# Performance work log

Measured on AMD Instinct MI355X. Metric: run time of the kernel, lower is better.

## Reference

```python
import jax, jax.numpy as jnp
import numpy as np

K = 10
SLOPE = 0.2
FEATS = [3, 64, 128, 256, 512, 1024]
MLP = [1024, 128, 64, 1]
B, N = 8, 2048


def setup_inputs() -> dict:
    key = jax.random.key(0)
    keys = jax.random.split(key, 32)
    inp = {"x": jax.random.normal(keys[0], (B, N, 3), dtype=jnp.float32)}
    ki = 1
    for i in range(5):
        fin, fout = 2 * FEATS[i], FEATS[i + 1]
        s = 1.0 / np.sqrt(fin)
        inp[f"w{i}"] = jax.random.uniform(keys[ki], (fin, fout), jnp.float32, -s, s); ki += 1
        inp[f"b{i}"] = jax.random.uniform(keys[ki], (fout,), jnp.float32, -s, s); ki += 1
    for i in range(3):
        fin, fout = MLP[i], MLP[i + 1]
        s = 1.0 / np.sqrt(fin)
        inp[f"m{i}w"] = jax.random.uniform(keys[ki], (fin, fout), jnp.float32, -s, s); ki += 1
        inp[f"m{i}b"] = jax.random.uniform(keys[ki], (fout,), jnp.float32, -s, s); ki += 1
    return inp


def _knn_idx(xb):
    # xb: [N, F]; squared euclidean distances, self included (dist 0)
    sq = jnp.sum(xb * xb, axis=-1)
    d2 = sq[:, None] + sq[None, :] - 2.0 * (xb @ xb.T)
    _, idx = jax.lax.top_k(-d2, K)  # [N, K] nearest (incl. self)
    return idx


def _edge_conv(x, W, b):
    # x: [B, N, F] -> [B, N, Fout]
    fin = x.shape[-1]
    W1, W2 = W[:fin], W[fin:]  # split concat([x_i, x_j - x_i]) @ W
    idx = jax.vmap(_knn_idx)(x)  # [B, N, K]
    x_j = jax.vmap(lambda xb, ib: xb[ib])(x, idx)  # [B, N, K, F]
    h_center = x @ W1 + b  # [B, N, Fout]
    diff = x_j - x[:, :, None, :]
    h = h_center[:, :, None, :] + jnp.einsum('bnkf,fo->bnko', diff, W2)
    h = jnp.where(h > 0, h, SLOPE * h)  # LeakyReLU(0.2)
    return jnp.max(h, axis=2)  # max aggregation over neighbors


def reference(x, w0, b0, w1, b1, w2, b2, w3, b3, w4, b4,
              m0w, m0b, m1w, m1b, m2w, m2b):
    ws = [(w0, b0), (w1, b1), (w2, b2), (w3, b3), (w4, b4)]
    h = x
    for W, b in ws:
        h = _edge_conv(h, W, b)
    g = jnp.max(h, axis=1)  # MaxPool1d(kernel=2048) -> global max over points: [B, 1024]
    g = g @ m0w + m0b
    g = g @ m1w + m1b
    g = g @ m2w + m2b
    return g  # [B, 1]
```

## Files before the change

### kernel.cpp

```cpp
#include <hip/hip_runtime.h>
#include <hip/hip_bf16.h>
#include <math.h>

#define BB 8
#define NN 2048
#define KK 10
#define BN (BB * NN)
#define HC 1024

typedef __attribute__((ext_vector_type(8))) short bf16x8;
typedef __attribute__((ext_vector_type(4))) float f32x4;

__device__ inline unsigned short f2bf(float f) {
    unsigned int u = __float_as_uint(f);
    unsigned int r = u + 0x7fffu + ((u >> 16) & 1u);
    return (unsigned short)(r >> 16);
}
__device__ inline float bf2f(unsigned short h) {
    return __uint_as_float((unsigned int)h << 16);
}

__device__ __forceinline__ void async16(const void* g, void* l) {
    __builtin_amdgcn_global_load_lds(
        (const __attribute__((address_space(1))) void*)g,
        (__attribute__((address_space(3))) void*)l, 16, 0, 0);
}

__global__ void xsplit3_kernel(const float* __restrict__ x,
                               unsigned short* __restrict__ hi,
                               unsigned short* __restrict__ lo,
                               float* __restrict__ sq) {
    int row = blockIdx.x * blockDim.x + threadIdx.x;
    if (row >= BN) return;
    unsigned short hbuf[32], lbuf[32];
#pragma unroll
    for (int f = 0; f < 32; ++f) { hbuf[f] = 0; lbuf[f] = 0; }
    float s = 0.f;
#pragma unroll
    for (int f = 0; f < 3; ++f) {
        float v = x[(size_t)row * 3 + f];
        s += v * v;
        unsigned short h = f2bf(v);
        hbuf[f] = h;
        lbuf[f] = f2bf(v - bf2f(h));
    }
    sq[row] = s;
#pragma unroll
    for (int f = 0; f < 32; f += 8) {
        *(uint4*)&hi[(size_t)row * 32 + f] = *(uint4*)&hbuf[f];
        *(uint4*)&lo[(size_t)row * 32 + f] = *(uint4*)&lbuf[f];
    }
}

__global__ __launch_bounds__(256) void xsplit_sq_kernel(
        const float* __restrict__ x, unsigned short* __restrict__ hi,
        unsigned short* __restrict__ lo, float* __restrict__ sq, int F) {
    int row = blockIdx.x * 4 + (threadIdx.x >> 6);
    int lane = threadIdx.x & 63;
    const float* xp = x + (size_t)row * F;
    float s = 0.f;
    for (int f = lane; f < F; f += 64) {
        float v = xp[f];
        unsigned short h = f2bf(v);
        hi[(size_t)row * F + f] = h;
        lo[(size_t)row * F + f] = f2bf(v - bf2f(h));
        s += v * v;
    }
#pragma unroll
    for (int off = 32; off > 0; off >>= 1) s += __shfl_down(s, off);
    if (lane == 0) sq[row] = s;
}

__global__ __launch_bounds__(256) void knn_gram_kernel(
        const unsigned short* __restrict__ xh, const unsigned short* __restrict__ xl,
        const float* __restrict__ sq, float* __restrict__ d2, int F, int qbase) {
    int b = blockIdx.z;
    int row0 = blockIdx.x * 128;
    int col0 = qbase + blockIdx.y * 128;
    const unsigned short* xhb = xh + (size_t)b * NN * F;
    const unsigned short* xlb = xl + (size_t)b * NN * F;
    const float* sqb = sq + (size_t)b * NN;

    __shared__ __align__(16) unsigned short AsB[4 * 128 * 32];
    unsigned short* Ah = AsB;
    unsigned short* Al = Ah + 128 * 32;
    unsigned short* Bh = Al + 128 * 32;
    unsigned short* Bl = Bh + 128 * 32;

    int tid = threadIdx.x;
    int lane = tid & 63;
    int wave = tid >> 6;
    int wr = (wave >> 1) * 64, wc = (wave & 1) * 64;
    int l15 = lane & 15, kq = lane >> 4;
    int rsub = lane >> 2;
    int csub = (((lane & 3) ^ ((lane >> 3) & 3))) * 8;
    int kqs = (kq ^ ((l15 >> 1) & 3)) * 8;

    f32x4 acc[4][4];
#pragma unroll
    for (int mt = 0; mt < 4; ++mt)
#pragma unroll
        for (int nt = 0; nt < 4; ++nt) acc[mt][nt] = (f32x4){0.f, 0.f, 0.f, 0.f};

    for (int kc = 0; kc < F; kc += 32) {
        __syncthreads();
#pragma unroll
        for (int j = 0; j < 2; ++j) {
            int row = wave * 32 + j * 16 + rsub;
            int dsto = wave * 1024 + j * 512;
            async16(xhb + (size_t)(row0 + row) * F + kc + csub, Ah + dsto);
            async16(xlb + (size_t)(row0 + row) * F + kc + csub, Al + dsto);
            async16(xhb + (size_t)(col0 + row) * F + kc + csub, Bh + dsto);
            async16(xlb + (size_t)(col0 + row) * F + kc + csub, Bl + dsto);
        }
        __syncthreads();
        bf16x8 bh[4], bl[4];
#pragma unroll
        for (int t = 0; t < 4; ++t) {
            bh[t] = *(const bf16x8*)&Bh[(wc + t * 16 + l15) * 32 + kqs];
            bl[t] = *(const bf16x8*)&Bl[(wc + t * 16 + l15) * 32 + kqs];
        }
#pragma unroll
        for (int mt = 0; mt < 4; ++mt) {
            bf16x8 ah = *(const bf16x8*)&Ah[(wr + mt * 16 + l15) * 32 + kqs];
            bf16x8 al = *(const bf16x8*)&Al[(wr + mt * 16 + l15) * 32 + kqs];
#pragma unroll
            for (int nt = 0; nt < 4; ++nt) {
                acc[mt][nt] = __builtin_amdgcn_mfma_f32_16x16x32_bf16(ah, bh[nt], acc[mt][nt], 0, 0, 0);
                acc[mt][nt] = __builtin_amdgcn_mfma_f32_16x16x32_bf16(al, bh[nt], acc[mt][nt], 0, 0, 0);
                acc[mt][nt] = __builtin_amdgcn_mfma_f32_16x16x32_bf16(ah, bl[nt], acc[mt][nt], 0, 0, 0);
            }
        }
    }
#pragma unroll
    for (int mt = 0; mt < 4; ++mt) {
        int rbase = row0 + wr + mt * 16 + kq * 4;
#pragma unroll
        for (int nt = 0; nt < 4; ++nt) {
            int lc = (col0 - qbase) + wc + nt * 16 + l15;
            float sqc = sqb[col0 + wc + nt * 16 + l15];
            f32x4 c = acc[mt][nt];
#pragma unroll
            for (int r = 0; r < 4; ++r) {
                float sqr = sqb[rbase + r];
                d2[((size_t)b * NN + rbase + r) * HC + lc] = (sqr + sqc) - 2.f * c[r];
            }
        }
    }
}

__global__ __launch_bounds__(256) void knn_select_kernel(
        const float* __restrict__ d2a, const float* __restrict__ d2b,
        int* __restrict__ idx) {
    int row = blockIdx.x * 4 + (threadIdx.x >> 6);
    int lane = threadIdx.x & 63;
    const float* ra = d2a + (size_t)row * HC;
    const float* rb = d2b + (size_t)row * HC;

    float4 v[8];
#pragma unroll
    for (int it = 0; it < 4; ++it) {
        v[it]     = *(const float4*)&ra[it * 256 + lane * 4];
        v[it + 4] = *(const float4*)&rb[it * 256 + lane * 4];
    }

    float bestd[KK];
    int besti[KK];
#pragma unroll
    for (int k = 0; k < KK; ++k) { bestd[k] = INFINITY; besti[k] = 0x7fffffff; }

#pragma unroll
    for (int it = 0; it < 8; ++it) {
        int cbase = ((it < 4) ? (it * 256) : (HC + (it - 4) * 256)) + lane * 4;
        float dv[4] = {v[it].x, v[it].y, v[it].z, v[it].w};
#pragma unroll
        for (int s4 = 0; s4 < 4; ++s4) {
            float d = dv[s4];
            if (d < bestd[KK - 1]) {
                bestd[KK - 1] = d;
                besti[KK - 1] = cbase + s4;
#pragma unroll
                for (int s = KK - 1; s > 0; --s) {
                    if (bestd[s] < bestd[s - 1]) {
                        float td = bestd[s]; bestd[s] = bestd[s - 1]; bestd[s - 1] = td;
                        int ti = besti[s]; besti[s] = besti[s - 1]; besti[s - 1] = ti;
                    }
                }
            }
        }
    }

    int h = 0;
    int mywin = 0;
    for (int s = 0; s < KK; ++s) {
        float dd = (h < KK) ? bestd[h] : INFINITY;
        int ii = (h < KK) ? besti[h] : 0x7fffffff;
        float d0 = dd; int i0 = ii;
#pragma unroll
        for (int off = 32; off > 0; off >>= 1) {
            float od = __shfl_xor(dd, off);
            int oi = __shfl_xor(ii, off);
            if (od < dd || (od == dd && oi < ii)) { dd = od; ii = oi; }
        }
        if (lane == s) mywin = ii;
        if (h < KK && i0 == ii && d0 == dd) h++;
    }
    if (lane < KK) idx[(size_t)row * KK + lane] = mywin;
}

__global__ void wsplit_kernel(const float* __restrict__ w, unsigned short* __restrict__ WT,
                              int fin, int fpad, int fout) {
    int i = blockIdx.x * blockDim.x + threadIdx.x;
    int total = 2 * fout * fpad;
    if (i >= total) return;
    int op = i % (2 * fout);
    int f = i / (2 * fout);
    float v = 0.f;
    if (f < fin) {
        if (op < fout) v = w[(size_t)f * fout + op] - w[(size_t)(fin + f) * fout + op];
        else v = w[(size_t)(fin + f) * fout + (op - fout)];
    }
    unsigned short h = f2bf(v);
    unsigned short l = f2bf(v - bf2f(h));
    WT[(size_t)op * (2 * fpad) + f] = h;
    WT[(size_t)op * (2 * fpad) + fpad + f] = l;
}

__global__ __launch_bounds__(256) void gemm2_mfma_kernel(
        const unsigned short* __restrict__ XSh, const unsigned short* __restrict__ XSl,
        const unsigned short* __restrict__ WT, const float* __restrict__ bias,
        float* __restrict__ Aout, float* __restrict__ Tout, int fin, int fout) {
    int m0 = blockIdx.x * 128;
    int n0 = blockIdx.y * 128;
    __shared__ __align__(16) unsigned short AsB[4 * 128 * 32];
    unsigned short* Ah = AsB;
    unsigned short* Al = Ah + 128 * 32;
    unsigned short* Bh = Al + 128 * 32;
    unsigned short* Bl = Bh + 128 * 32;

    int tid = threadIdx.x;
    int lane = tid & 63;
    int wave = tid >> 6;
    int wr = (wave >> 1) * 64, wc = (wave & 1) * 64;
    int l15 = lane & 15, kq = lane >> 4;
    int rsub = lane >> 2;
    int csub = (((lane & 3) ^ ((lane >> 3) & 3))) * 8;
    int kqs = (kq ^ ((l15 >> 1) & 3)) * 8;
    int w2f = 2 * fin;

    f32x4 acc[4][4];
#pragma unroll
    for (int mt = 0; mt < 4; ++mt)
#pragma unroll
        for (int nt = 0; nt < 4; ++nt) acc[mt][nt] = (f32x4){0.f, 0.f, 0.f, 0.f};

    for (int kc = 0; kc < fin; kc += 32) {
        __syncthreads();
#pragma unroll
        for (int j = 0; j < 2; ++j) {
            int row = wave * 32 + j * 16 + rsub;
            int dsto = wave * 1024 + j * 512;
            async16(XSh + (size_t)(m0 + row) * fin + kc + csub, Ah + dsto);
            async16(XSl + (size_t)(m0 + row) * fin + kc + csub, Al + dsto);
            async16(WT + (size_t)(n0 + row) * w2f + kc + csub, Bh + dsto);
            async16(WT + (size_t)(n0 + row) * w2f + fin + kc + csub, Bl + dsto);
        }
        __syncthreads();
        bf16x8 bh[4], bl[4];
#pragma unroll
        for (int t = 0; t < 4; ++t) {
            bh[t] = *(const bf16x8*)&Bh[(wc + t * 16 + l15) * 32 + kqs];
            bl[t] = *(const bf16x8*)&Bl[(wc + t * 16 + l15) * 32 + kqs];
        }
#pragma unroll
        for (int mt = 0; mt < 4; ++mt) {
            bf16x8 ah = *(const bf16x8*)&Ah[(wr + mt * 16 + l15) * 32 + kqs];
            bf16x8 al = *(const bf16x8*)&Al[(wr + mt * 16 + l15) * 32 + kqs];
#pragma unroll
            for (int nt = 0; nt < 4; ++nt) {
                acc[mt][nt] = __builtin_amdgcn_mfma_f32_16x16x32_bf16(ah, bh[nt], acc[mt][nt], 0, 0, 0);
                acc[mt][nt] = __builtin_amdgcn_mfma_f32_16x16x32_bf16(al, bh[nt], acc[mt][nt], 0, 0, 0);
                acc[mt][nt] = __builtin_amdgcn_mfma_f32_16x16x32_bf16(ah, bl[nt], acc[mt][nt], 0, 0, 0);
            }
        }
    }
#pragma unroll
    for (int mt = 0; mt < 4; ++mt) {
        int mbase = m0 + wr + mt * 16 + kq * 4;
#pragma unroll
        for (int nt = 0; nt < 4; ++nt) {
            int oc = n0 + wc + nt * 16 + l15;
            f32x4 c = acc[mt][nt];
            if (oc < fout) {
                float bv = bias[oc];
#pragma unroll
                for (int r = 0; r < 4; ++r)
                    Aout[(size_t)(mbase + r) * fout + oc] = c[r] + bv;
            } else {
                int o2 = oc - fout;
#pragma unroll
                for (int r = 0; r < 4; ++r)
                    Tout[(size_t)(mbase + r) * fout + o2] = c[r];
            }
        }
    }
}

__global__ __launch_bounds__(256) void gathermax_kernel(
        const float* __restrict__ A, const float* __restrict__ T,
        const int* __restrict__ idx, float* __restrict__ out,
        int shift, int total4b) {
    int b = blockIdx.y;
    int sh4 = shift - 2;
    int fm4 = (1 << sh4) - 1;
    int fout = 1 << shift;
    int stride = gridDim.x * 256;
    const float* Tb = T + ((size_t)b << 11) * fout;
    for (int e4 = blockIdx.x * 256 + threadIdx.x; e4 < total4b; e4 += stride) {
        int pnl = e4 >> sh4;
        int o = (e4 & fm4) * 4;
        int pn = (b << 11) + pnl;
        const int* ip = idx + (size_t)pn * KK;
        float4 m = {-INFINITY, -INFINITY, -INFINITY, -INFINITY};
#pragma unroll
        for (int k = 0; k < KK; ++k) {
            int j = ip[k];
            float4 t = *(const float4*)&Tb[(size_t)j * fout + o];
            m.x = fmaxf(m.x, t.x); m.y = fmaxf(m.y, t.y);
            m.z = fmaxf(m.z, t.z); m.w = fmaxf(m.w, t.w);
        }
        float4 a = *(const float4*)&A[(size_t)pn * fout + o];
        float4 h;
        h.x = a.x + m.x; h.y = a.y + m.y; h.z = a.z + m.z; h.w = a.w + m.w;
        h.x = h.x > 0.f ? h.x : 0.2f * h.x;
        h.y = h.y > 0.f ? h.y : 0.2f * h.y;
        h.z = h.z > 0.f ? h.z : 0.2f * h.z;
        h.w = h.w > 0.f ? h.w : 0.2f * h.w;
        *(float4*)&out[(size_t)pn * fout + o] = h;
    }
}

__global__ void gmax1_kernel(const float* __restrict__ h, float* __restrict__ gp) {
    int b = blockIdx.y;
    int chunk = blockIdx.z;
    int o = blockIdx.x * 256 + threadIdx.x;
    const float* hp = h + ((size_t)b * NN + chunk * 128) * 1024 + o;
    float m = -INFINITY;
    for (int n = 0; n < 128; ++n) m = fmaxf(m, hp[(size_t)n * 1024]);
    gp[((size_t)chunk * BB + b) * 1024 + o] = m;
}
__global__ void gmax2_kernel(const float* __restrict__ gp, float* __restrict__ g) {
    int b = blockIdx.y;
    int o = blockIdx.x * 256 + threadIdx.x;
    float m = -INFINITY;
    for (int c = 0; c < 16; ++c) m = fmaxf(m, gp[((size_t)c * BB + b) * 1024 + o]);
    g[(size_t)b * 1024 + o] = m;
}

__global__ __launch_bounds__(128) void mlp_kernel(const float* __restrict__ g,
                                                  const float* __restrict__ m0w, const float* __restrict__ m0b,
                                                  const float* __restrict__ m1w, const float* __restrict__ m1b,
                                                  const float* __restrict__ m2w, const float* __restrict__ m2b,
                                                  float* __restrict__ out) {
    __shared__ float gs[1024];
    __shared__ float h1[128];
    __shared__ float h2[64];
    int b = blockIdx.x, t = threadIdx.x;
    for (int i = t; i < 1024; i += 128) gs[i] = g[(size_t)b * 1024 + i];
    __syncthreads();
    float s = m0b[t];
    for (int f = 0; f < 1024; ++f) s += gs[f] * m0w[(size_t)f * 128 + t];
    h1[t] = s;
    __syncthreads();
    if (t < 64) {
        float s2 = m1b[t];
        for (int f = 0; f < 128; ++f) s2 += h1[f] * m1w[(size_t)f * 64 + t];
        h2[t] = s2;
    }
    __syncthreads();
    if (t == 0) {
        float s3 = m2b[0];
        for (int f = 0; f < 64; ++f) s3 += h2[f] * m2w[f];
        out[b] = s3;
    }
}

extern "C" void kernel_launch(void* const* d_in, const int* in_sizes, int n_in,
                              void* d_out, int out_size, void* d_ws, size_t ws_size,
                              hipStream_t stream) {
    const float* x0 = (const float*)d_in[0];
    const float* w[5], * bi[5];
    for (int i = 0; i < 5; ++i) { w[i] = (const float*)d_in[1 + 2 * i]; bi[i] = (const float*)d_in[2 + 2 * i]; }
    const float* m0w = (const float*)d_in[11]; const float* m0b = (const float*)d_in[12];
    const float* m1w = (const float*)d_in[13]; const float* m1b = (const float*)d_in[14];
    const float* m2w = (const float*)d_in[15]; const float* m2b = (const float*)d_in[16];

    float* X0 = (float*)d_ws;
    float* X1 = X0 + (size_t)BN * 1024;
    float* T  = X1 + (size_t)BN * 1024;
    float* SQ = T  + (size_t)BN * 1024;
    int*   IDX = (int*)(SQ + BN);
    float* G  = (float*)(IDX + (size_t)BN * KK);
    unsigned short* XSh = (unsigned short*)(G + (size_t)BB * 1024);
    unsigned short* XSl = XSh + (size_t)BN * 512;
    unsigned short* WT  = XSl + (size_t)BN * 512;

    float* GP = T;

    const int fouts[5] = {64, 128, 256, 512, 1024};
    const int shifts[5] = {6, 7, 8, 9, 10};
    const float* cur = x0;
    int fin = 3;
    float* bufs[2] = {X0, X1};

    for (int l = 0; l < 5; ++l) {
        int fout = fouts[l];
        float* nxt = bufs[l & 1];
        int Fg = (l == 0) ? 32 : fin;

        if (l == 0) {
            xsplit3_kernel<<<(BN + 255) / 256, 256, 0, stream>>>(cur, XSh, XSl, SQ);
        } else {
            xsplit_sq_kernel<<<BN / 4, 256, 0, stream>>>(cur, XSh, XSl, SQ, fin);
        }

        float* D2a = T;
        float* D2b = nxt;
        dim3 gg2(NN / 128, HC / 128, BB);
        knn_gram_kernel<<<gg2, 256, 0, stream>>>(XSh, XSl, SQ, D2a, Fg, 0);
        knn_gram_kernel<<<gg2, 256, 0, stream>>>(XSh, XSl, SQ, D2b, Fg, HC);
        knn_select_kernel<<<BN / 4, 256, 0, stream>>>(D2a, D2b, IDX);

        int nw = 2 * fout * Fg;
        wsplit_kernel<<<(nw + 255) / 256, 256, 0, stream>>>(w[l], WT, fin, Fg, fout);
        dim3 gg(BN / 128, (2 * fout) / 128);
        gemm2_mfma_kernel<<<gg, 256, 0, stream>>>(XSh, XSl, WT, bi[l], nxt, T, Fg, fout);

        dim3 gmg(256, BB);
        gathermax_kernel<<<gmg, 256, 0, stream>>>(nxt, T, IDX, nxt, shifts[l], (NN * fout) / 4);

        cur = nxt;
        fin = fout;
    }

    dim3 x1(1024 / 256, BB, 16);
    gmax1_kernel<<<x1, 256, 0, stream>>>(cur, GP);
    dim3 x2(1024 / 256, BB);
    gmax2_kernel<<<x2, 256, 0, stream>>>(GP, G);

    mlp_kernel<<<BB, 128, 0, stream>>>(G, m0w, m0b, m1w, m1b, m2w, m2b, (float*)d_out);
}
```

Baseline: 1.146 ms.

## Exploit distance-matrix symmetry: compute upper-triangle tiles and write transposed copies

The separate gram launches for the two column halves are merged into one launch. That launch covers only the 136 upper-triangular 128x128 tiles per batch instead of all 256. Each off-diagonal tile writes its result directly and also writes the transpose, staged through padded LDS to keep the global stores coalesced. This roughly halves the MFMA work of the split-bf16 distance computation. In exchange the off-diagonal tiles take on an extra LDS transpose pass with extra barriers, and the triangular index decode loop adds a little per-block work.

```diff
diff --git a/kernel.cpp b/kernel.cpp
--- a/kernel.cpp
+++ b/kernel.cpp
@@ -73,19 +73,24 @@
 
 __global__ __launch_bounds__(256) void knn_gram_kernel(
         const unsigned short* __restrict__ xh, const unsigned short* __restrict__ xl,
-        const float* __restrict__ sq, float* __restrict__ d2, int F, int qbase) {
-    int b = blockIdx.z;
-    int row0 = blockIdx.x * 128;
-    int col0 = qbase + blockIdx.y * 128;
+        const float* __restrict__ sq, float* __restrict__ d2a,
+        float* __restrict__ d2b, int F) {
+    int b = blockIdx.y;
+    int t = blockIdx.x, ti = 0;
+    while (t >= 16 - ti) { t -= 16 - ti; ti++; }
+    int tj = ti + t;
+    int row0 = ti * 128;
+    int col0 = tj * 128;
     const unsigned short* xhb = xh + (size_t)b * NN * F;
     const unsigned short* xlb = xl + (size_t)b * NN * F;
     const float* sqb = sq + (size_t)b * NN;
 
-    __shared__ __align__(16) unsigned short AsB[4 * 128 * 32];
-    unsigned short* Ah = AsB;
+    __shared__ __align__(16) unsigned char smem_raw[33024];
+    unsigned short* Ah = (unsigned short*)smem_raw;
     unsigned short* Al = Ah + 128 * 32;
     unsigned short* Bh = Al + 128 * 32;
     unsigned short* Bl = Bh + 128 * 32;
+    float* LT = (float*)smem_raw;
 
     int tid = threadIdx.x;
     int lane = tid & 63;
@@ -116,9 +121,9 @@
         __syncthreads();
         bf16x8 bh[4], bl[4];
 #pragma unroll
-        for (int t = 0; t < 4; ++t) {
-            bh[t] = *(const bf16x8*)&Bh[(wc + t * 16 + l15) * 32 + kqs];
-            bl[t] = *(const bf16x8*)&Bl[(wc + t * 16 + l15) * 32 + kqs];
+        for (int t4 = 0; t4 < 4; ++t4) {
+            bh[t4] = *(const bf16x8*)&Bh[(wc + t4 * 16 + l15) * 32 + kqs];
+            bl[t4] = *(const bf16x8*)&Bl[(wc + t4 * 16 + l15) * 32 + kqs];
         }
 #pragma unroll
         for (int mt = 0; mt < 4; ++mt) {
@@ -132,18 +137,52 @@
             }
         }
     }
-#pragma unroll
-    for (int mt = 0; mt < 4; ++mt) {
-        int rbase = row0 + wr + mt * 16 + kq * 4;
-#pragma unroll
-        for (int nt = 0; nt < 4; ++nt) {
-            int lc = (col0 - qbase) + wc + nt * 16 + l15;
-            float sqc = sqb[col0 + wc + nt * 16 + l15];
-            f32x4 c = acc[mt][nt];
-#pragma unroll
-            for (int r = 0; r < 4; ++r) {
-                float sqr = sqb[rbase + r];
-                d2[((size_t)b * NN + rbase + r) * HC + lc] = (sqr + sqc) - 2.f * c[r];
+    {
+        float* dst = (col0 < HC) ? d2a : d2b;
+        int lc0 = col0 & (HC - 1);
+#pragma unroll
+        for (int mt = 0; mt < 4; ++mt) {
+            int rbase = row0 + wr + mt * 16 + kq * 4;
+#pragma unroll
+            for (int nt = 0; nt < 4; ++nt) {
+                int cc = wc + nt * 16 + l15;
+                float sqc = sqb[col0 + cc];
+#pragma unroll
+                for (int r = 0; r < 4; ++r) {
+                    float v = (sqb[rbase + r] + sqc) - 2.f * acc[mt][nt][r];
+                    acc[mt][nt][r] = v;
+                    dst[((size_t)b * NN + rbase + r) * HC + lc0 + cc] = v;
+                }
+            }
+        }
+    }
+    if (ti != tj) {
+        float* mdst = (row0 < HC) ? d2a : d2b;
+        int mc0 = row0 & (HC - 1);
+#pragma unroll
+        for (int h = 0; h < 2; ++h) {
+            __syncthreads();
+            if ((wave & 1) == h) {
+#pragma unroll
+                for (int mt = 0; mt < 4; ++mt)
+#pragma unroll
+                    for (int nt = 0; nt < 4; ++nt)
+#pragma unroll
+                        for (int r = 0; r < 4; ++r)
+                            LT[(nt * 16 + l15) * 129 + (wr + mt * 16 + kq * 4 + r)] =
+                                acc[mt][nt][r];
+            }
+            __syncthreads();
+#pragma unroll
+            for (int it = 0; it < 8; ++it) {
+                int v = tid + it * 256;
+                int lr = v >> 5, c4 = v & 31;
+                float4 val;
+                val.x = LT[lr * 129 + c4 * 4];
+                val.y = LT[lr * 129 + c4 * 4 + 1];
+                val.z = LT[lr * 129 + c4 * 4 + 2];
+                val.w = LT[lr * 129 + c4 * 4 + 3];
+                *(float4*)&mdst[((size_t)b * NN + col0 + h * 64 + lr) * HC + mc0 + c4 * 4] = val;
             }
         }
     }
@@ -426,9 +465,8 @@
 
         float* D2a = T;
         float* D2b = nxt;
-        dim3 gg2(NN / 128, HC / 128, BB);
-        knn_gram_kernel<<<gg2, 256, 0, stream>>>(XSh, XSl, SQ, D2a, Fg, 0);
-        knn_gram_kernel<<<gg2, 256, 0, stream>>>(XSh, XSl, SQ, D2b, Fg, HC);
+        dim3 gg2(136, BB);
+        knn_gram_kernel<<<gg2, 256, 0, stream>>>(XSh, XSl, SQ, D2a, D2b, Fg);
         knn_select_kernel<<<BN / 4, 256, 0, stream>>>(D2a, D2b, IDX);
 
         int nw = 2 * fout * Fg;
```

Measured after the change: 1.054 ms. -8.0%, faster.
